# Performance work log

Hardware: AMD Instinct MI355X
Metric: run time of the kernel (lower is better)

Reference implementation:

```python
import jax, jax.numpy as jnp
import numpy as np

INPUT_SIZE = 784
HIDDEN_SIZE = 256
NUM_CLASSES = 10
BATCH = 32768


def setup_inputs() -> dict:
    key = jax.random.key(0)
    k_x, k_w1, k_b1, k_w2, k_b2 = jax.random.split(key, 5)
    return {
        "x": jax.random.normal(k_x, (BATCH, INPUT_SIZE), dtype=jnp.float32),
        "fc1_weight": jax.random.normal(k_w1, (HIDDEN_SIZE, INPUT_SIZE), dtype=jnp.float32),
        "fc1_bias": jax.random.normal(k_b1, (HIDDEN_SIZE,), dtype=jnp.float32),
        "fc2_weight": jax.random.normal(k_w2, (NUM_CLASSES, HIDDEN_SIZE), dtype=jnp.float32),
        "fc2_bias": jax.random.normal(k_b2, (NUM_CLASSES,), dtype=jnp.float32),
    }


def reference(x, fc1_weight, fc1_bias, fc2_weight, fc2_bias):
    # hidden = x @ W1^T + b1, ReLU
    hidden = jnp.einsum("bi,hi->bh", x, fc1_weight) + fc1_bias
    activated = jnp.maximum(hidden, 0.0)
    # output = activated @ W2^T + b2
    logits = jnp.einsum("bh,ch->bc", activated, fc2_weight) + fc2_bias
    return jax.nn.softmax(logits, axis=-1)
```

## Files before the change

### kernel.cpp

```cpp
#include <hip/hip_runtime.h>
#include <math.h>

#define BATCH_N   32768
#define IN_F      784
#define HID_F     256
#define NCLS      10
#define BM        64
#define NTHREADS  512

typedef __attribute__((ext_vector_type(8)))  short short8;
typedef __attribute__((ext_vector_type(4)))  float f32x4;
typedef __attribute__((ext_vector_type(16))) float f32x16;

#define WS_W1H 0
#define WS_W1L 401408

union S8U { short8 s; uint4 u; };

__device__ __forceinline__ void cvt8(float4 a, float4 b, short8* hi, short8* lo) {
    const unsigned M = 0xFFFF0000u;
    const unsigned ux = __float_as_uint(a.x), uy = __float_as_uint(a.y),
                   uz = __float_as_uint(a.z), uw = __float_as_uint(a.w),
                   vx = __float_as_uint(b.x), vy = __float_as_uint(b.y),
                   vz = __float_as_uint(b.z), vw = __float_as_uint(b.w);
    S8U h, l;
    h.u.x = (ux >> 16) | (uy & M);
    h.u.y = (uz >> 16) | (uw & M);
    h.u.z = (vx >> 16) | (vy & M);
    h.u.w = (vz >> 16) | (vw & M);
    const float rx = a.x - __uint_as_float(ux & M);
    const float ry = a.y - __uint_as_float(uy & M);
    const float rz = a.z - __uint_as_float(uz & M);
    const float rw = a.w - __uint_as_float(uw & M);
    const float sx = b.x - __uint_as_float(vx & M);
    const float sy = b.y - __uint_as_float(vy & M);
    const float sz = b.z - __uint_as_float(vz & M);
    const float sw_ = b.w - __uint_as_float(vw & M);
    l.u.x = (__float_as_uint(rx) >> 16) | (__float_as_uint(ry) & M);
    l.u.y = (__float_as_uint(rz) >> 16) | (__float_as_uint(rw) & M);
    l.u.z = (__float_as_uint(sx) >> 16) | (__float_as_uint(sy) & M);
    l.u.w = (__float_as_uint(sz) >> 16) | (__float_as_uint(sw_) & M);
    *hi = h.s; *lo = l.s;
}

__device__ __forceinline__ void cvt8v(f32x4 a, f32x4 b, short8* hi, short8* lo) {
    float4 fa = make_float4(a[0], a[1], a[2], a[3]);
    float4 fb = make_float4(b[0], b[1], b[2], b[3]);
    cvt8(fa, fb, hi, lo);
}

__global__ __launch_bounds__(256)
void prep_w1_kernel(const float* __restrict__ w1, char* __restrict__ ws) {
    const int s    = blockIdx.x * 256 + threadIdx.x;
    const int lane = s & 63, ct = (s >> 6) & 7, kt = s >> 9;
    const int n    = ct * 32 + (lane & 31);
    const int k0   = kt * 16 + (lane >> 5) * 8;
    const float* p = w1 + (size_t)n * IN_F + k0;
    const float4 a = *(const float4*)p;
    const float4 b = *(const float4*)(p + 4);
    short8 hi, lo;
    cvt8(a, b, &hi, &lo);
    *(short8*)(ws + WS_W1H + (size_t)s * 16) = hi;
    *(short8*)(ws + WS_W1L + (size_t)s * 16) = lo;
}

__device__ __forceinline__ short8 gload_s8(const void* p) {
    short8 r;
    asm volatile("global_load_dwordx4 %0, %1, off" : "=v"(r) : "v"(p));
    return r;
}
__device__ __forceinline__ f32x4 gload_f4(const float* p) {
    f32x4 r;
    asm volatile("global_load_dwordx4 %0, %1, off" : "=v"(r) : "v"(p));
    return r;
}

#define MFMA32(A, B, C) __builtin_amdgcn_mfma_f32_32x32x16_bf16((A), (B), (C), 0, 0, 0)

__global__ __launch_bounds__(NTHREADS, 2)
void mlp_mfma_kernel(const float* __restrict__ x,
                     const char*  __restrict__ wsb,
                     const float* __restrict__ b1,
                     const float* __restrict__ w2,
                     const float* __restrict__ b2,
                     float* __restrict__ out)
{
    __shared__ union {
        char  stage[2][28672];
        float hid[64 * 256];
    } sm;

    const int tid   = threadIdx.x;
    const int lane  = tid & 63;
    const int wv    = tid >> 6;
    const int l31   = lane & 31;
    const int khalf = lane >> 5;
    const int row0  = blockIdx.x * BM;

    const int srow  = tid & 63;
    const int sktl  = (wv < 7) ? wv : 6;
    const float* xs = x + (size_t)(row0 + srow) * IN_F + sktl * 16;
    const int ssw   = (srow >> 2) & 1;
    const int swo0  = sktl * 2048 + srow * 32 + (0 ^ ssw) * 16;
    const int swo1  = sktl * 2048 + srow * 32 + (1 ^ ssw) * 16;

    const int asw = (l31 >> 2) & 1;
    const int aro = l31 * 32 + ((khalf ^ asw) << 4);

    const char* bhp = wsb + WS_W1H + ((size_t)wv * 64 + lane) * 16;
    const char* blp = wsb + WS_W1L + ((size_t)wv * 64 + lane) * 16;

    f32x16 acc0, acc1;
    #pragma unroll
    for (int r = 0; r < 16; ++r) { acc0[r] = 0.f; acc1[r] = 0.f; }

    f32x4 s0 = gload_f4(xs), s1 = gload_f4(xs + 4),
          s2 = gload_f4(xs + 8), s3 = gload_f4(xs + 12);
    short8 bh0, bl0, bh1, bl1;
    bh0 = gload_s8(bhp);
    bl0 = gload_s8(blp);
    asm volatile("s_waitcnt vmcnt(2)" ::: "memory");
    __builtin_amdgcn_sched_barrier(0);
    if (wv < 7) {
        short8 h0, l0, h1, l1;
        cvt8v(s0, s1, &h0, &l0);
        cvt8v(s2, s3, &h1, &l1);
        char* st = sm.stage[0];
        *(short8*)(st + swo0)         = h0;
        *(short8*)(st + 14336 + swo0) = l0;
        *(short8*)(st + swo1)         = h1;
        *(short8*)(st + 14336 + swo1) = l1;
    }
    asm volatile("s_waitcnt lgkmcnt(0)" ::: "memory");
    __builtin_amdgcn_sched_barrier(0);
    __builtin_amdgcn_s_barrier();
    __builtin_amdgcn_sched_barrier(0);

    #pragma unroll
    for (int g = 0; g < 7; ++g) {
        const char* bufr = sm.stage[g & 1];
        #pragma unroll
        for (int t = 0; t < 7; ++t) {
            const int kt = g * 7 + t;
            if (kt < 48) {
                const char* pbh = bhp + (size_t)(kt + 1) * 8192;
                const char* pbl = blp + (size_t)(kt + 1) * 8192;
                if (kt & 1) { bh0 = gload_s8(pbh); bl0 = gload_s8(pbl); }
                else        { bh1 = gload_s8(pbh); bl1 = gload_s8(pbl); }
            }
            if (g < 6 && t == 4) {
                const float* sp = xs + (g + 1) * 112;
                s0 = gload_f4(sp);      s1 = gload_f4(sp + 4);
                s2 = gload_f4(sp + 8);  s3 = gload_f4(sp + 12);
            }
            if (g < 6 && (t == 4 || t == 5)) {
                asm volatile("s_waitcnt vmcnt(6)" ::: "memory");
            } else if (kt == 48) {
                asm volatile("s_waitcnt vmcnt(0)" ::: "memory");
            } else {
                asm volatile("s_waitcnt vmcnt(2)" ::: "memory");
            }
            __builtin_amdgcn_sched_barrier(0);
            const short8 ah0 = *(const short8*)(bufr + t * 2048 + aro);
            const short8 al0 = *(const short8*)(bufr + 14336 + t * 2048 + aro);
            const short8 ah1 = *(const short8*)(bufr + t * 2048 + aro + 1024);
            const short8 al1 = *(const short8*)(bufr + 14336 + t * 2048 + aro + 1024);
            __builtin_amdgcn_s_setprio(1);
            if (kt & 1) {
                acc0 = MFMA32(ah0, bh1, acc0);
                acc0 = MFMA32(al0, bh1, acc0);
                acc0 = MFMA32(ah0, bl1, acc0);
                acc1 = MFMA32(ah1, bh1, acc1);
                acc1 = MFMA32(al1, bh1, acc1);
                acc1 = MFMA32(ah1, bl1, acc1);
            } else {
                acc0 = MFMA32(ah0, bh0, acc0);
                acc0 = MFMA32(al0, bh0, acc0);
                acc0 = MFMA32(ah0, bl0, acc0);
                acc1 = MFMA32(ah1, bh0, acc1);
                acc1 = MFMA32(al1, bh0, acc1);
                acc1 = MFMA32(ah1, bl0, acc1);
            }
            __builtin_amdgcn_s_setprio(0);
            __builtin_amdgcn_sched_barrier(0);
        }
        if (g < 6) {
            if (wv < 7) {
                short8 h0, l0, h1, l1;
                cvt8v(s0, s1, &h0, &l0);
                cvt8v(s2, s3, &h1, &l1);
                char* st = sm.stage[(g + 1) & 1];
                *(short8*)(st + swo0)         = h0;
                *(short8*)(st + 14336 + swo0) = l0;
                *(short8*)(st + swo1)         = h1;
                *(short8*)(st + 14336 + swo1) = l1;
            }
            asm volatile("s_waitcnt lgkmcnt(0)" ::: "memory");
            __builtin_amdgcn_sched_barrier(0);
            __builtin_amdgcn_s_barrier();
            __builtin_amdgcn_sched_barrier(0);
        }
    }

    __syncthreads();
    {
        const int col = wv * 32 + l31;
        const float bv = b1[col];
        #pragma unroll
        for (int reg = 0; reg < 16; ++reg) {
            const int rowb = (reg & 3) + 8 * (reg >> 2) + 4 * khalf;
            sm.hid[rowb * 256 + (col ^ ((rowb & 7) << 2))] =
                fmaxf(acc0[reg] + bv, 0.f);
            const int rowc = 32 + rowb;
            sm.hid[rowc * 256 + (col ^ ((rowc & 7) << 2))] =
                fmaxf(acc1[reg] + bv, 0.f);
        }
    }
    __syncthreads();

    const int rl    = tid >> 3;
    const int slice = tid & 7;
    const int sw2   = (rl & 7) << 2;
    float lg[NCLS];
    #pragma unroll
    for (int k = 0; k < NCLS; ++k) lg[k] = 0.f;
    #pragma unroll
    for (int i = 0; i < 8; ++i) {
        const int col = slice * 32 + i * 4;
        const float4 h = *(const float4*)(sm.hid + rl * 256 + (col ^ sw2));
        #pragma unroll
        for (int k = 0; k < NCLS; ++k) {
            const float4 w = *(const float4*)(w2 + k * HID_F + col);
            lg[k] += h.x * w.x + h.y * w.y + h.z * w.z + h.w * w.w;
        }
    }
    #pragma unroll
    for (int k = 0; k < NCLS; ++k) {
        float v = lg[k];
        v += __shfl_xor(v, 1);
        v += __shfl_xor(v, 2);
        v += __shfl_xor(v, 4);
        lg[k] = v + b2[k];
    }
    float mx = -1e30f;
    #pragma unroll
    for (int k = 0; k < NCLS; ++k) mx = fmaxf(mx, lg[k]);
    float s = 0.f;
    #pragma unroll
    for (int k = 0; k < NCLS; ++k) { lg[k] = __expf(lg[k] - mx); s += lg[k]; }
    const float inv = 1.f / s;
    const float va = (slice & 4)
        ? ((slice & 2) ? ((slice & 1) ? lg[7] : lg[6]) : ((slice & 1) ? lg[5] : lg[4]))
        : ((slice & 2) ? ((slice & 1) ? lg[3] : lg[2]) : ((slice & 1) ? lg[1] : lg[0]));
    const float vb = (slice & 1) ? lg[9] : lg[8];
    float* o = out + (size_t)(row0 + rl) * NCLS;
    o[slice] = va * inv;
    if (slice < 2) o[8 + slice] = vb * inv;
}

extern "C" void kernel_launch(void* const* d_in, const int* in_sizes, int n_in,
                              void* d_out, int out_size, void* d_ws, size_t ws_size,
                              hipStream_t stream)
{
    const float* x  = (const float*)d_in[0];
    const float* w1 = (const float*)d_in[1];
    const float* b1 = (const float*)d_in[2];
    const float* w2 = (const float*)d_in[3];
    const float* b2 = (const float*)d_in[4];
    float* out = (float*)d_out;

    hipLaunchKernelGGL(prep_w1_kernel, dim3(98), dim3(256), 0, stream,
                       w1, (char*)d_ws);
    hipLaunchKernelGGL(mlp_mfma_kernel, dim3(BATCH_N / BM), dim3(NTHREADS), 0, stream,
                       x, (const char*)d_ws, b1, w2, b2, out);
}
```

Before: 213.2 us.

## Double row tile to 128 with four accumulators per wave and restaged K loop

Each block now covers 128 batch rows instead of 64, so each wave keeps four 32x32 accumulators and every W1 fragment loaded from global memory is reused across twice as many rows. The x staging is reorganised so all 512 threads load a 64-wide K slab per round (12 rounds plus a tail), replacing the 7x7 loop over 112-wide groups. The epilogue runs in two 64-row halves through the shared hidden buffer, with rotated column reads to spread LDS bank access. The costs are higher register pressure from 64 accumulator floats per lane, the risk of losing 2 blocks per CU, and half as many blocks in the grid.

Measured after the change: 187.7 us. -12.0%, faster.

```diff
diff --git a/kernel.cpp b/kernel.cpp
--- a/kernel.cpp
+++ b/kernel.cpp
@@ -5,7 +5,7 @@
 #define IN_F      784
 #define HID_F     256
 #define NCLS      10
-#define BM        64
+#define BM        128
 #define NTHREADS  512
 
 typedef __attribute__((ext_vector_type(8)))  short short8;
@@ -77,6 +77,80 @@
 
 #define MFMA32(A, B, C) __builtin_amdgcn_mfma_f32_32x32x16_bf16((A), (B), (C), 0, 0, 0)
 
+#define MFMA_KT(BUF, KTL, BH, BL)                                              \
+    {                                                                          \
+        __builtin_amdgcn_s_setprio(1);                                         \
+        _Pragma("unroll")                                                      \
+        for (int rt = 0; rt < 4; ++rt) {                                       \
+            const short8 ah = *(const short8*)((BUF) + (KTL) * 4096 + rt * 1024 + aro); \
+            const short8 al = *(const short8*)((BUF) + 16384 + (KTL) * 4096 + rt * 1024 + aro); \
+            acc[rt] = MFMA32(ah, BH, acc[rt]);                                 \
+            acc[rt] = MFMA32(al, BH, acc[rt]);                                 \
+            acc[rt] = MFMA32(ah, BL, acc[rt]);                                 \
+        }                                                                      \
+        __builtin_amdgcn_s_setprio(0);                                         \
+    }
+
+#define XISSUE4(G) do {                                                        \
+        s0 = gload_f4(xs + ((G) + 1) * 64 + sq * 8);                           \
+        s1 = gload_f4(xs + ((G) + 1) * 64 + sq * 8 + 4);                       \
+        s2 = gload_f4(xs + ((G) + 1) * 64 + 32 + sq * 8);                      \
+        s3 = gload_f4(xs + ((G) + 1) * 64 + 32 + sq * 8 + 4);                  \
+    } while (0)
+#define XISSUET() do {                                                         \
+        s0 = gload_f4(xs + 768 + (sq & 1) * 8);                                \
+        s1 = gload_f4(xs + 768 + (sq & 1) * 8 + 4);                            \
+    } while (0)
+#define CVT4W(BW) do {                                                         \
+        short8 h0, l0, h1, l1;                                                 \
+        cvt8v(s0, s1, &h0, &l0);                                               \
+        cvt8v(s2, s3, &h1, &l1);                                               \
+        *(short8*)((BW) + wo0)         = h0;                                   \
+        *(short8*)((BW) + 16384 + wo0) = l0;                                   \
+        *(short8*)((BW) + wo1)         = h1;                                   \
+        *(short8*)((BW) + 16384 + wo1) = l1;                                   \
+    } while (0)
+#define CVTTW(BW) do {                                                         \
+        short8 h0, l0;                                                         \
+        cvt8v(s0, s1, &h0, &l0);                                               \
+        if (sq < 2) {                                                          \
+            *(short8*)((BW) + wot)         = h0;                               \
+            *(short8*)((BW) + 16384 + wot) = l0;                               \
+        }                                                                      \
+    } while (0)
+
+#define ROUND(G, W1, XI, CVTW)                                                 \
+    {                                                                          \
+        const char* bufr = sm.stage[(G) & 1];                                  \
+        char* bufw = sm.stage[((G) + 1) & 1];                                  \
+        bhO = gload_s8(bhp + (size_t)(4 * (G) + 1) * 8192);                    \
+        blO = gload_s8(blp + (size_t)(4 * (G) + 1) * 8192);                    \
+        asm volatile("s_waitcnt vmcnt(2)" ::: "memory");                       \
+        __builtin_amdgcn_sched_barrier(0);                                     \
+        MFMA_KT(bufr, 0, bhE, blE);                                            \
+        bhE = gload_s8(bhp + (size_t)(4 * (G) + 2) * 8192);                    \
+        blE = gload_s8(blp + (size_t)(4 * (G) + 2) * 8192);                    \
+        XI;                                                                    \
+        asm volatile(W1 ::: "memory");                                         \
+        __builtin_amdgcn_sched_barrier(0);                                     \
+        MFMA_KT(bufr, 1, bhO, blO);                                            \
+        bhO = gload_s8(bhp + (size_t)(4 * (G) + 3) * 8192);                    \
+        blO = gload_s8(blp + (size_t)(4 * (G) + 3) * 8192);                    \
+        asm volatile(W1 ::: "memory");                                         \
+        __builtin_amdgcn_sched_barrier(0);                                     \
+        MFMA_KT(bufr, 2, bhE, blE);                                            \
+        bhE = gload_s8(bhp + (size_t)(4 * (G) + 4) * 8192);                    \
+        blE = gload_s8(blp + (size_t)(4 * (G) + 4) * 8192);                    \
+        asm volatile("s_waitcnt vmcnt(2)" ::: "memory");                       \
+        __builtin_amdgcn_sched_barrier(0);                                     \
+        MFMA_KT(bufr, 3, bhO, blO);                                            \
+        CVTW(bufw);                                                            \
+        asm volatile("s_waitcnt lgkmcnt(0)" ::: "memory");                     \
+        __builtin_amdgcn_sched_barrier(0);                                     \
+        __builtin_amdgcn_s_barrier();                                          \
+        __builtin_amdgcn_sched_barrier(0);                                     \
+    }
+
 __global__ __launch_bounds__(NTHREADS, 2)
 void mlp_mfma_kernel(const float* __restrict__ x,
                      const char*  __restrict__ wsb,
@@ -86,7 +160,7 @@
                      float* __restrict__ out)
 {
     __shared__ union {
-        char  stage[2][28672];
+        char  stage[2][32768];
         float hid[64 * 256];
     } sm;
 
@@ -97,12 +171,13 @@
     const int khalf = lane >> 5;
     const int row0  = blockIdx.x * BM;
 
-    const int srow  = tid & 63;
-    const int sktl  = (wv < 7) ? wv : 6;
-    const float* xs = x + (size_t)(row0 + srow) * IN_F + sktl * 16;
-    const int ssw   = (srow >> 2) & 1;
-    const int swo0  = sktl * 2048 + srow * 32 + (0 ^ ssw) * 16;
-    const int swo1  = sktl * 2048 + srow * 32 + (1 ^ ssw) * 16;
+    const int sr  = tid >> 2;
+    const int sq  = tid & 3;
+    const float* xs = x + (size_t)(row0 + sr) * IN_F;
+    const int ssw = (sr >> 2) & 1;
+    const int wo0 = (sq >> 1) * 4096 + sr * 32 + (((sq & 1) ^ ssw) << 4);
+    const int wo1 = wo0 + 8192;
+    const int wot = sr * 32 + ((sq ^ ssw) << 4);
 
     const int asw = (l31 >> 2) & 1;
     const int aro = l31 * 32 + ((khalf ^ asw) << 4);
@@ -110,152 +185,106 @@
     const char* bhp = wsb + WS_W1H + ((size_t)wv * 64 + lane) * 16;
     const char* blp = wsb + WS_W1L + ((size_t)wv * 64 + lane) * 16;
 
-    f32x16 acc0, acc1;
+    f32x16 acc[4];
     #pragma unroll
-    for (int r = 0; r < 16; ++r) { acc0[r] = 0.f; acc1[r] = 0.f; }
-
-    f32x4 s0 = gload_f4(xs), s1 = gload_f4(xs + 4),
-          s2 = gload_f4(xs + 8), s3 = gload_f4(xs + 12);
-    short8 bh0, bl0, bh1, bl1;
-    bh0 = gload_s8(bhp);
-    bl0 = gload_s8(blp);
+    for (int rt = 0; rt < 4; ++rt)
+        #pragma unroll
+        for (int r = 0; r < 16; ++r) acc[rt][r] = 0.f;
+
+    short8 bhE, blE, bhO, blO;
+    f32x4 s0, s1, s2, s3;
+
+    s0 = gload_f4(xs + sq * 8);
+    s1 = gload_f4(xs + sq * 8 + 4);
+    s2 = gload_f4(xs + 32 + sq * 8);
+    s3 = gload_f4(xs + 32 + sq * 8 + 4);
+    bhE = gload_s8(bhp);
+    blE = gload_s8(blp);
     asm volatile("s_waitcnt vmcnt(2)" ::: "memory");
     __builtin_amdgcn_sched_barrier(0);
-    if (wv < 7) {
-        short8 h0, l0, h1, l1;
-        cvt8v(s0, s1, &h0, &l0);
-        cvt8v(s2, s3, &h1, &l1);
-        char* st = sm.stage[0];
-        *(short8*)(st + swo0)         = h0;
-        *(short8*)(st + 14336 + swo0) = l0;
-        *(short8*)(st + swo1)         = h1;
-        *(short8*)(st + 14336 + swo1) = l1;
-    }
+    CVT4W(sm.stage[0]);
     asm volatile("s_waitcnt lgkmcnt(0)" ::: "memory");
     __builtin_amdgcn_sched_barrier(0);
     __builtin_amdgcn_s_barrier();
     __builtin_amdgcn_sched_barrier(0);
 
-    #pragma unroll
-    for (int g = 0; g < 7; ++g) {
-        const char* bufr = sm.stage[g & 1];
-        #pragma unroll
-        for (int t = 0; t < 7; ++t) {
-            const int kt = g * 7 + t;
-            if (kt < 48) {
-                const char* pbh = bhp + (size_t)(kt + 1) * 8192;
-                const char* pbl = blp + (size_t)(kt + 1) * 8192;
-                if (kt & 1) { bh0 = gload_s8(pbh); bl0 = gload_s8(pbl); }
-                else        { bh1 = gload_s8(pbh); bl1 = gload_s8(pbl); }
-            }
-            if (g < 6 && t == 4) {
-                const float* sp = xs + (g + 1) * 112;
-                s0 = gload_f4(sp);      s1 = gload_f4(sp + 4);
-                s2 = gload_f4(sp + 8);  s3 = gload_f4(sp + 12);
-            }
-            if (g < 6 && (t == 4 || t == 5)) {
-                asm volatile("s_waitcnt vmcnt(6)" ::: "memory");
-            } else if (kt == 48) {
-                asm volatile("s_waitcnt vmcnt(0)" ::: "memory");
-            } else {
-                asm volatile("s_waitcnt vmcnt(2)" ::: "memory");
-            }
-            __builtin_amdgcn_sched_barrier(0);
-            const short8 ah0 = *(const short8*)(bufr + t * 2048 + aro);
-            const short8 al0 = *(const short8*)(bufr + 14336 + t * 2048 + aro);
-            const short8 ah1 = *(const short8*)(bufr + t * 2048 + aro + 1024);
-            const short8 al1 = *(const short8*)(bufr + 14336 + t * 2048 + aro + 1024);
-            __builtin_amdgcn_s_setprio(1);
-            if (kt & 1) {
-                acc0 = MFMA32(ah0, bh1, acc0);
-                acc0 = MFMA32(al0, bh1, acc0);
-                acc0 = MFMA32(ah0, bl1, acc0);
-                acc1 = MFMA32(ah1, bh1, acc1);
-                acc1 = MFMA32(al1, bh1, acc1);
-                acc1 = MFMA32(ah1, bl1, acc1);
-            } else {
-                acc0 = MFMA32(ah0, bh0, acc0);
-                acc0 = MFMA32(al0, bh0, acc0);
-                acc0 = MFMA32(ah0, bl0, acc0);
-                acc1 = MFMA32(ah1, bh0, acc1);
-                acc1 = MFMA32(al1, bh0, acc1);
-                acc1 = MFMA32(ah1, bl0, acc1);
-            }
-            __builtin_amdgcn_s_setprio(0);
-            __builtin_amdgcn_sched_barrier(0);
-        }
-        if (g < 6) {
-            if (wv < 7) {
-                short8 h0, l0, h1, l1;
-                cvt8v(s0, s1, &h0, &l0);
-                cvt8v(s2, s3, &h1, &l1);
-                char* st = sm.stage[(g + 1) & 1];
-                *(short8*)(st + swo0)         = h0;
-                *(short8*)(st + 14336 + swo0) = l0;
-                *(short8*)(st + swo1)         = h1;
-                *(short8*)(st + 14336 + swo1) = l1;
-            }
-            asm volatile("s_waitcnt lgkmcnt(0)" ::: "memory");
-            __builtin_amdgcn_sched_barrier(0);
-            __builtin_amdgcn_s_barrier();
-            __builtin_amdgcn_sched_barrier(0);
-        }
+    ROUND(0,  "s_waitcnt vmcnt(6)", XISSUE4(0),  CVT4W)
+    ROUND(1,  "s_waitcnt vmcnt(6)", XISSUE4(1),  CVT4W)
+    ROUND(2,  "s_waitcnt vmcnt(6)", XISSUE4(2),  CVT4W)
+    ROUND(3,  "s_waitcnt vmcnt(6)", XISSUE4(3),  CVT4W)
+    ROUND(4,  "s_waitcnt vmcnt(6)", XISSUE4(4),  CVT4W)
+    ROUND(5,  "s_waitcnt vmcnt(6)", XISSUE4(5),  CVT4W)
+    ROUND(6,  "s_waitcnt vmcnt(6)", XISSUE4(6),  CVT4W)
+    ROUND(7,  "s_waitcnt vmcnt(6)", XISSUE4(7),  CVT4W)
+    ROUND(8,  "s_waitcnt vmcnt(6)", XISSUE4(8),  CVT4W)
+    ROUND(9,  "s_waitcnt vmcnt(6)", XISSUE4(9),  CVT4W)
+    ROUND(10, "s_waitcnt vmcnt(6)", XISSUE4(10), CVT4W)
+    ROUND(11, "s_waitcnt vmcnt(4)", XISSUET(),   CVTTW)
+    {
+        asm volatile("s_waitcnt vmcnt(0)" ::: "memory");
+        __builtin_amdgcn_sched_barrier(0);
+        MFMA_KT(sm.stage[0], 0, bhE, blE);
     }
-
-    __syncthreads();
-    {
-        const int col = wv * 32 + l31;
-        const float bv = b1[col];
-        #pragma unroll
-        for (int reg = 0; reg < 16; ++reg) {
-            const int rowb = (reg & 3) + 8 * (reg >> 2) + 4 * khalf;
-            sm.hid[rowb * 256 + (col ^ ((rowb & 7) << 2))] =
-                fmaxf(acc0[reg] + bv, 0.f);
-            const int rowc = 32 + rowb;
-            sm.hid[rowc * 256 + (col ^ ((rowc & 7) << 2))] =
-                fmaxf(acc1[reg] + bv, 0.f);
-        }
-    }
-    __syncthreads();
 
     const int rl    = tid >> 3;
     const int slice = tid & 7;
     const int sw2   = (rl & 7) << 2;
-    float lg[NCLS];
+
     #pragma unroll
-    for (int k = 0; k < NCLS; ++k) lg[k] = 0.f;
-    #pragma unroll
-    for (int i = 0; i < 8; ++i) {
-        const int col = slice * 32 + i * 4;
-        const float4 h = *(const float4*)(sm.hid + rl * 256 + (col ^ sw2));
+    for (int half = 0; half < 2; ++half) {
+        __syncthreads();
+        {
+            const int col = wv * 32 + l31;
+            const float bv = b1[col];
+            #pragma unroll
+            for (int rr = 0; rr < 2; ++rr) {
+                const int rt = half * 2 + rr;
+                #pragma unroll
+                for (int reg = 0; reg < 16; ++reg) {
+                    const int row = rr * 32 + (reg & 3) + 8 * (reg >> 2) + 4 * khalf;
+                    sm.hid[row * 256 + (col ^ ((row & 7) << 2))] =
+                        fmaxf(acc[rt][reg] + bv, 0.f);
+                }
+            }
+        }
+        __syncthreads();
+        float lg[NCLS];
+        #pragma unroll
+        for (int k = 0; k < NCLS; ++k) lg[k] = 0.f;
+        #pragma unroll
+        for (int i = 0; i < 8; ++i) {
+            const int ii  = ((i + slice) & 7) * 4;
+            const int col = slice * 32 + ii;
+            const float4 h = *(const float4*)(sm.hid + rl * 256 + (slice * 32 + (ii ^ sw2)));
+            #pragma unroll
+            for (int k = 0; k < NCLS; ++k) {
+                const float4 w = *(const float4*)(w2 + k * HID_F + col);
+                lg[k] += h.x * w.x + h.y * w.y + h.z * w.z + h.w * w.w;
+            }
+        }
         #pragma unroll
         for (int k = 0; k < NCLS; ++k) {
-            const float4 w = *(const float4*)(w2 + k * HID_F + col);
-            lg[k] += h.x * w.x + h.y * w.y + h.z * w.z + h.w * w.w;
+            float v = lg[k];
+            v += __shfl_xor(v, 1);
+            v += __shfl_xor(v, 2);
+            v += __shfl_xor(v, 4);
+            lg[k] = v + b2[k];
         }
+        float mx = -1e30f;
+        #pragma unroll
+        for (int k = 0; k < NCLS; ++k) mx = fmaxf(mx, lg[k]);
+        float s = 0.f;
+        #pragma unroll
+        for (int k = 0; k < NCLS; ++k) { lg[k] = __expf(lg[k] - mx); s += lg[k]; }
+        const float inv = 1.f / s;
+        const float va = (slice & 4)
+            ? ((slice & 2) ? ((slice & 1) ? lg[7] : lg[6]) : ((slice & 1) ? lg[5] : lg[4]))
+            : ((slice & 2) ? ((slice & 1) ? lg[3] : lg[2]) : ((slice & 1) ? lg[1] : lg[0]));
+        const float vb = (slice & 1) ? lg[9] : lg[8];
+        float* o = out + (size_t)(row0 + half * 64 + rl) * NCLS;
+        o[slice] = va * inv;
+        if (slice < 2) o[8 + slice] = vb * inv;
     }
-    #pragma unroll
-    for (int k = 0; k < NCLS; ++k) {
-        float v = lg[k];
-        v += __shfl_xor(v, 1);
-        v += __shfl_xor(v, 2);
-        v += __shfl_xor(v, 4);
-        lg[k] = v + b2[k];
-    }
-    float mx = -1e30f;
-    #pragma unroll
-    for (int k = 0; k < NCLS; ++k) mx = fmaxf(mx, lg[k]);
-    float s = 0.f;
-    #pragma unroll
-    for (int k = 0; k < NCLS; ++k) { lg[k] = __expf(lg[k] - mx); s += lg[k]; }
-    const float inv = 1.f / s;
-    const float va = (slice & 4)
-        ? ((slice & 2) ? ((slice & 1) ? lg[7] : lg[6]) : ((slice & 1) ? lg[5] : lg[4]))
-        : ((slice & 2) ? ((slice & 1) ? lg[3] : lg[2]) : ((slice & 1) ? lg[1] : lg[0]));
-    const float vb = (slice & 1) ? lg[9] : lg[8];
-    float* o = out + (size_t)(row0 + rl) * NCLS;
-    o[slice] = va * inv;
-    if (slice < 2) o[8 + slice] = vb * inv;
 }
 
 extern "C" void kernel_launch(void* const* d_in, const int* in_sizes, int n_in,
```
